# Performance work log

Hardware: AMD Instinct MI355X
Metric: run time of the kernel (lower is better)

## Reference

```python
import jax, jax.numpy as jnp
import numpy as np

N_NODES = 50000
N_EDGES = 800000
D_IN = 64
D_OUT = 64


def setup_inputs() -> dict:
    key = jax.random.key(0)
    k1, k2, k3, k4, k5, k6 = jax.random.split(key, 6)
    stdv = 1.0 / np.sqrt(D_OUT)
    return {
        "X": jax.random.normal(k1, (N_NODES, D_IN), dtype=jnp.float32),
        "edge_src": jax.random.randint(k2, (N_EDGES,), 0, N_NODES, dtype=jnp.int32),
        "edge_dst": jax.random.randint(k3, (N_EDGES,), 0, N_NODES, dtype=jnp.int32),
        "edge_weight": jax.random.uniform(k4, (N_EDGES,), dtype=jnp.float32),
        "weight": jax.random.uniform(k5, (D_IN, D_OUT), jnp.float32, -stdv, stdv),
        "b": jax.random.uniform(k6, (D_OUT,), jnp.float32, -stdv, stdv),
    }


def reference(X, edge_src, edge_dst, edge_weight, weight, b):
    # support = X @ W                        [N, D_OUT]
    support = jnp.dot(X, weight)
    # spmm: out[d] = sum_{e: dst(e)=d} w_e * support[src(e)]
    messages = edge_weight[:, None] * support[edge_src]  # [E, D_OUT]
    output = jax.ops.segment_sum(messages, edge_dst, num_segments=N_NODES)
    return output + b
```

## Files before the change

kernel.cpp:

```cpp
#include <hip/hip_runtime.h>
#include <hip/hip_bf16.h>

#define N_NODES 50000
#define N_EDGES 800000
#define DIM     64
#define CAP     64

#define GEMM_BLOCKS ((N_NODES + 63) / 64)
#define FILL_BLOCKS ((N_EDGES / 4 + 255) / 256)

#define WS_SUPPORT  0
#define WS_CURSOR   6400000
#define WS_BUCKET   9600000

__device__ inline unsigned bf16_hi(float f) {
    const unsigned u = __float_as_uint(f);
    return (u + 0x7fffu + ((u >> 16) & 1u)) & 0xffff0000u;
}

__global__ __launch_bounds__(256) void fused_gemm_fill_kernel(
        const float* __restrict__ X,
        const float* __restrict__ W,
        ushort* __restrict__ support,
        const int*   __restrict__ edge_src,
        const int*   __restrict__ edge_dst,
        const float* __restrict__ edge_weight,
        int*      __restrict__ cursor,
        unsigned* __restrict__ bucket) {
    const int bid = blockIdx.x >> 1;
    const int tid = threadIdx.x;

    if (blockIdx.x & 1) {
        const int base = (bid * 256 + tid) * 4;
        if (base < N_EDGES) {
            const int4   d = *(const int4*)  &edge_dst[base];
            const int4   s = *(const int4*)  &edge_src[base];
            const float4 w = *(const float4*)&edge_weight[base];
            const unsigned e0 = bf16_hi(w.x) | (unsigned)s.x;
            const unsigned e1 = bf16_hi(w.y) | (unsigned)s.y;
            const unsigned e2 = bf16_hi(w.z) | (unsigned)s.z;
            const unsigned e3 = bf16_hi(w.w) | (unsigned)s.w;
            const int p0 = atomicAdd(&cursor[d.x << 4], 1);
            const int p1 = atomicAdd(&cursor[d.y << 4], 1);
            const int p2 = atomicAdd(&cursor[d.z << 4], 1);
            const int p3 = atomicAdd(&cursor[d.w << 4], 1);
            if (p0 < CAP) bucket[d.x * CAP + p0] = e0;
            if (p1 < CAP) bucket[d.y * CAP + p1] = e1;
            if (p2 < CAP) bucket[d.z * CAP + p2] = e2;
            if (p3 < CAP) bucket[d.w * CAP + p3] = e3;
        }
        return;
    }

    __shared__ float sX[64 * 68];
    __shared__ float sW[64 * 64];
    const int rowBase = bid * 64;

    #pragma unroll
    for (int i = 0; i < 4; ++i) {
        const int q   = tid + 256 * i;
        const int row = q >> 4;
        const int c4  = q & 15;
        float4 v = make_float4(0.f, 0.f, 0.f, 0.f);
        if (rowBase + row < N_NODES)
            v = *(const float4*)&X[(rowBase + row) * DIM + c4 * 4];
        *(float4*)&sX[row * 68 + c4 * 4] = v;
    }
    #pragma unroll
    for (int i = 0; i < 4; ++i) {
        const int q   = tid + 256 * i;
        const int row = q >> 4;
        const int c4  = q & 15;
        *(float4*)&sW[row * 64 + c4 * 4] = *(const float4*)&W[row * DIM + c4 * 4];
    }
    __syncthreads();

    const int tx = tid & 15;
    const int ty = tid >> 4;
    float acc[4][4];
    #pragma unroll
    for (int i = 0; i < 4; ++i)
        #pragma unroll
        for (int j = 0; j < 4; ++j) acc[i][j] = 0.f;

    #pragma unroll
    for (int k4 = 0; k4 < 16; ++k4) {
        float4 xv[4], wv[4];
        #pragma unroll
        for (int i = 0; i < 4; ++i)
            xv[i] = *(const float4*)&sX[(ty * 4 + i) * 68 + k4 * 4];
        #pragma unroll
        for (int kk = 0; kk < 4; ++kk)
            wv[kk] = *(const float4*)&sW[(k4 * 4 + kk) * 64 + tx * 4];
        #pragma unroll
        for (int i = 0; i < 4; ++i) {
            #pragma unroll
            for (int kk = 0; kk < 4; ++kk) {
                const float f = ((const float*)&xv[i])[kk];
                acc[i][0] += f * wv[kk].x;
                acc[i][1] += f * wv[kk].y;
                acc[i][2] += f * wv[kk].z;
                acc[i][3] += f * wv[kk].w;
            }
        }
    }

    #pragma unroll
    for (int i = 0; i < 4; ++i) {
        const int r = rowBase + ty * 4 + i;
        if (r < N_NODES) {
            ushort4 v;
            v.x = __hip_bfloat16_raw(__float2bfloat16(acc[i][0])).x;
            v.y = __hip_bfloat16_raw(__float2bfloat16(acc[i][1])).x;
            v.z = __hip_bfloat16_raw(__float2bfloat16(acc[i][2])).x;
            v.w = __hip_bfloat16_raw(__float2bfloat16(acc[i][3])).x;
            *(ushort4*)&support[r * DIM + tx * 4] = v;
        }
    }
}

__global__ __launch_bounds__(256) void gather_kernel(const int*      __restrict__ cursor,
                                                     const unsigned* __restrict__ bucket,
                                                     const ushort*   __restrict__ support,
                                                     const float*    __restrict__ b,
                                                     float* __restrict__ out) {
    const int node = blockIdx.x * 4 + (threadIdx.x >> 6);
    const int lane = threadIdx.x & 63;
    if (node >= N_NODES) return;

    int cnt = cursor[node << 4];
    if (cnt > CAP) cnt = CAP;
    const unsigned ent = bucket[node * CAP + lane];

    float acc = 0.f;
    int j = 0;
    for (; j + 4 <= cnt; j += 4) {
        const unsigned e0 = __shfl(ent, j);
        const unsigned e1 = __shfl(ent, j + 1);
        const unsigned e2 = __shfl(ent, j + 2);
        const unsigned e3 = __shfl(ent, j + 3);
        const float v0 = __uint_as_float((unsigned)support[(e0 & 0xffffu) * DIM + lane] << 16);
        const float v1 = __uint_as_float((unsigned)support[(e1 & 0xffffu) * DIM + lane] << 16);
        const float v2 = __uint_as_float((unsigned)support[(e2 & 0xffffu) * DIM + lane] << 16);
        const float v3 = __uint_as_float((unsigned)support[(e3 & 0xffffu) * DIM + lane] << 16);
        acc += __uint_as_float(e0 & 0xffff0000u) * v0;
        acc += __uint_as_float(e1 & 0xffff0000u) * v1;
        acc += __uint_as_float(e2 & 0xffff0000u) * v2;
        acc += __uint_as_float(e3 & 0xffff0000u) * v3;
    }
    for (; j < cnt; ++j) {
        const unsigned e = __shfl(ent, j);
        const float    v = __uint_as_float((unsigned)support[(e & 0xffffu) * DIM + lane] << 16);
        acc += __uint_as_float(e & 0xffff0000u) * v;
    }
    out[node * DIM + lane] = acc + b[lane];
}

extern "C" void kernel_launch(void* const* d_in, const int* in_sizes, int n_in,
                              void* d_out, int out_size, void* d_ws, size_t ws_size,
                              hipStream_t stream) {
    const float* X           = (const float*)d_in[0];
    const int*   edge_src    = (const int*)  d_in[1];
    const int*   edge_dst    = (const int*)  d_in[2];
    const float* edge_weight = (const float*)d_in[3];
    const float* W           = (const float*)d_in[4];
    const float* b           = (const float*)d_in[5];
    float*       out         = (float*)d_out;

    char* ws = (char*)d_ws;
    ushort*   support = (ushort*)  (ws + WS_SUPPORT);
    int*      cursor  = (int*)     (ws + WS_CURSOR);
    unsigned* bucket  = (unsigned*)(ws + WS_BUCKET);

    hipMemsetAsync(cursor, 0, N_NODES * 16 * sizeof(int), stream);

    hipLaunchKernelGGL(fused_gemm_fill_kernel, dim3(GEMM_BLOCKS + FILL_BLOCKS),
                       dim3(256), 0, stream,
                       X, W, support, edge_src, edge_dst, edge_weight,
                       cursor, bucket);

    hipLaunchKernelGGL(gather_kernel, dim3(N_NODES / 4), dim3(256), 0, stream,
                       cursor, bucket, support, b, out);
}
```

Measured before the change: 139.2 us.

## Merge edge bucketing into every GEMM block to overlap atomics with FMA work

Each block now performs both the 64-row GEMM tile and the bucket fill for its 1024 edges, instead of alternating dedicated GEMM and fill blocks. Edge loads are issued before the shared-memory staging, the cursor atomics are issued after the barrier, and the bucket stores happen after the FMA loop. The aim is to hide atomic and global-load latency behind the matrix compute and halve the grid size. The cost is more live registers per thread and a longer per-block critical path, which could reduce occupancy.

```diff
diff --git a/kernel.cpp b/kernel.cpp
--- a/kernel.cpp
+++ b/kernel.cpp
@@ -7,7 +7,6 @@
 #define CAP     64
 
 #define GEMM_BLOCKS ((N_NODES + 63) / 64)
-#define FILL_BLOCKS ((N_EDGES / 4 + 255) / 256)
 
 #define WS_SUPPORT  0
 #define WS_CURSOR   6400000
@@ -27,34 +26,23 @@
         const float* __restrict__ edge_weight,
         int*      __restrict__ cursor,
         unsigned* __restrict__ bucket) {
-    const int bid = blockIdx.x >> 1;
+    const int bid = blockIdx.x;
     const int tid = threadIdx.x;
-
-    if (blockIdx.x & 1) {
-        const int base = (bid * 256 + tid) * 4;
-        if (base < N_EDGES) {
-            const int4   d = *(const int4*)  &edge_dst[base];
-            const int4   s = *(const int4*)  &edge_src[base];
-            const float4 w = *(const float4*)&edge_weight[base];
-            const unsigned e0 = bf16_hi(w.x) | (unsigned)s.x;
-            const unsigned e1 = bf16_hi(w.y) | (unsigned)s.y;
-            const unsigned e2 = bf16_hi(w.z) | (unsigned)s.z;
-            const unsigned e3 = bf16_hi(w.w) | (unsigned)s.w;
-            const int p0 = atomicAdd(&cursor[d.x << 4], 1);
-            const int p1 = atomicAdd(&cursor[d.y << 4], 1);
-            const int p2 = atomicAdd(&cursor[d.z << 4], 1);
-            const int p3 = atomicAdd(&cursor[d.w << 4], 1);
-            if (p0 < CAP) bucket[d.x * CAP + p0] = e0;
-            if (p1 < CAP) bucket[d.y * CAP + p1] = e1;
-            if (p2 < CAP) bucket[d.z * CAP + p2] = e2;
-            if (p3 < CAP) bucket[d.w * CAP + p3] = e3;
-        }
-        return;
-    }
 
     __shared__ float sX[64 * 68];
     __shared__ float sW[64 * 64];
     const int rowBase = bid * 64;
+
+    const int  base      = (bid * 256 + tid) * 4;
+    const bool haveEdges = (base < N_EDGES);
+    int4   d = make_int4(0, 0, 0, 0);
+    int4   s = make_int4(0, 0, 0, 0);
+    float4 w = make_float4(0.f, 0.f, 0.f, 0.f);
+    if (haveEdges) {
+        d = *(const int4*)  &edge_dst[base];
+        s = *(const int4*)  &edge_src[base];
+        w = *(const float4*)&edge_weight[base];
+    }
 
     #pragma unroll
     for (int i = 0; i < 4; ++i) {
@@ -73,7 +61,21 @@
         const int c4  = q & 15;
         *(float4*)&sW[row * 64 + c4 * 4] = *(const float4*)&W[row * DIM + c4 * 4];
     }
+
+    const unsigned e0 = bf16_hi(w.x) | (unsigned)s.x;
+    const unsigned e1 = bf16_hi(w.y) | (unsigned)s.y;
+    const unsigned e2 = bf16_hi(w.z) | (unsigned)s.z;
+    const unsigned e3 = bf16_hi(w.w) | (unsigned)s.w;
+
     __syncthreads();
+
+    int p0 = 0, p1 = 0, p2 = 0, p3 = 0;
+    if (haveEdges) {
+        p0 = atomicAdd(&cursor[d.x << 4], 1);
+        p1 = atomicAdd(&cursor[d.y << 4], 1);
+        p2 = atomicAdd(&cursor[d.z << 4], 1);
+        p3 = atomicAdd(&cursor[d.w << 4], 1);
+    }
 
     const int tx = tid & 15;
     const int ty = tid >> 4;
@@ -103,6 +105,13 @@
                 acc[i][3] += f * wv[kk].w;
             }
         }
+    }
+
+    if (haveEdges) {
+        if (p0 < CAP) bucket[d.x * CAP + p0] = e0;
+        if (p1 < CAP) bucket[d.y * CAP + p1] = e1;
+        if (p2 < CAP) bucket[d.z * CAP + p2] = e2;
+        if (p3 < CAP) bucket[d.w * CAP + p3] = e3;
     }
 
     #pragma unroll
@@ -174,7 +183,7 @@
 
     hipMemsetAsync(cursor, 0, N_NODES * 16 * sizeof(int), stream);
 
-    hipLaunchKernelGGL(fused_gemm_fill_kernel, dim3(GEMM_BLOCKS + FILL_BLOCKS),
+    hipLaunchKernelGGL(fused_gemm_fill_kernel, dim3(GEMM_BLOCKS),
                        dim3(256), 0, stream,
                        X, W, support, edge_src, edge_dst, edge_weight,
                        cursor, bucket);
```

Result: slower. 154.5 us (+10.9%).
